# Kernel optimization log

Measured on AMD Instinct MI355X. Metric: run time of the kernel, lower is better.

Reference implementation:

```python
import jax, jax.numpy as jnp
import numpy as np

LN_EPS = 1e-5


def setup_inputs() -> dict:
    key = jax.random.key(0)
    k1, k2, k3, k4, k5, k6 = jax.random.split(key, 6)
    B, S, P = 4, 4096, 16          # batch, seq_len, max_n_bytes
    LR, D = 256, 1024              # lowrank_dim, embedding_dim
    # byte ids in [-1, 255]; -1 marks missing bytes
    bytes_ids = jax.random.randint(k1, (B, S, P), -1, 256)
    byte_table = jax.random.normal(k2, (256, LR), dtype=jnp.float32) * 0.02
    pos_emb = jax.random.normal(k3, (P, LR, LR), dtype=jnp.float32)
    W_up = jax.random.normal(k4, (D, LR), dtype=jnp.float32) * 0.02
    b_up = jnp.zeros((D,), dtype=jnp.float32)
    ln_gamma = jnp.ones((D,), dtype=jnp.float32)
    ln_beta = jnp.zeros((D,), dtype=jnp.float32)
    return {
        "bytes_ids": bytes_ids,
        "byte_table": byte_table,
        "pos_emb": pos_emb,
        "W_up": W_up,
        "b_up": b_up,
        "ln_gamma": ln_gamma,
        "ln_beta": ln_beta,
    }


def reference(bytes_ids, byte_table, pos_emb, W_up, b_up, ln_gamma, ln_beta):
    # bytes_ids: [B, S, P] int, -1 => missing byte
    missing = bytes_ids == -1                             # [B,S,P]
    ids = jnp.where(missing, 0, bytes_ids)
    be = byte_table[ids]                                  # [B,S,P,LR] gather
    # per-position small matmul: pos_emb[p] applied to each byte embedding
    emb = jnp.einsum('pij,bspi->bspj', pos_emb, be)       # [B,S,P,LR]
    emb = jnp.where(missing[..., None], 0.0, emb)         # mask missing bytes
    emb = emb.sum(axis=-2)                                # [B,S,LR]
    x = emb @ W_up.T + b_up                               # [B,S,D]
    # layernorm
    mu = x.mean(axis=-1, keepdims=True)
    var = jnp.mean(jnp.square(x - mu), axis=-1, keepdims=True)
    return (x - mu) * jax.lax.rsqrt(var + LN_EPS) * ln_gamma + ln_beta
```

## Files before the change

### kernel.cpp

```cpp
#include <hip/hip_runtime.h>
#include <stdint.h>

#define PP     16
#define LRDIM  256
#define DDIM   1024
#define LN_EPS 1e-5f

typedef __attribute__((ext_vector_type(8))) short  short8;
typedef __attribute__((ext_vector_type(4))) float  f32x4;

__device__ __forceinline__ uint32_t bf16_rne(float f) {
    uint32_t u = __builtin_bit_cast(uint32_t, f);
    return (u + 0x7fffu + ((u >> 16) & 1u)) >> 16;
}
__device__ __forceinline__ float bf_lo(uint32_t u) {
    return __builtin_bit_cast(float, u << 16);
}
__device__ __forceinline__ float bf_hi(uint32_t u) {
    return __builtin_bit_cast(float, u & 0xffff0000u);
}

__global__ __launch_bounds__(256) void k_table2b(const float* __restrict__ bt,
                                                 const float* __restrict__ pe,
                                                 unsigned short* __restrict__ t2b) {
    const int p  = blockIdx.x >> 6;
    const int c0 = (blockIdx.x & 63) * 4;
    const int j  = threadIdx.x;
    const float* pep = pe + (size_t)p * LRDIM * LRDIM;
    float a0 = 0.f, a1 = 0.f, a2 = 0.f, a3 = 0.f;
    for (int i = 0; i < LRDIM; ++i) {
        float v = pep[i * LRDIM + j];
        a0 += v * bt[(c0 + 0) * LRDIM + i];
        a1 += v * bt[(c0 + 1) * LRDIM + i];
        a2 += v * bt[(c0 + 2) * LRDIM + i];
        a3 += v * bt[(c0 + 3) * LRDIM + i];
    }
    t2b[(size_t)((p * 256) + c0 + 0) * LRDIM + j] = (unsigned short)bf16_rne(a0);
    t2b[(size_t)((p * 256) + c0 + 1) * LRDIM + j] = (unsigned short)bf16_rne(a1);
    t2b[(size_t)((p * 256) + c0 + 2) * LRDIM + j] = (unsigned short)bf16_rne(a2);
    t2b[(size_t)((p * 256) + c0 + 3) * LRDIM + j] = (unsigned short)bf16_rne(a3);
}

__global__ __launch_bounds__(256) void k_wblk(const float* __restrict__ W,
                                              uint4* __restrict__ wb) {
    const int gt  = blockIdx.x * 256 + threadIdx.x;
    const int l   = gt & 63;
    const int ks  = (gt >> 6) & 7;
    const int nfg = gt >> 9;
    const int n   = nfg * 16 + (l & 15);
    const int k   = ks * 32 + (l >> 4) * 8;
    const float* src = W + (size_t)n * LRDIM + k;
    uint32_t r[4];
#pragma unroll
    for (int q = 0; q < 4; ++q) {
        uint32_t lo = bf16_rne(src[2 * q + 0]);
        uint32_t hi = bf16_rne(src[2 * q + 1]);
        r[q] = lo | (hi << 16);
    }
    wb[gt] = make_uint4(r[0], r[1], r[2], r[3]);
}

__global__ __launch_bounds__(256, 2) void k_main(const int* __restrict__ ids,
                                                 const unsigned short* __restrict__ t2b,
                                                 const uint4* __restrict__ wb,
                                                 const float* __restrict__ b_up,
                                                 const float* __restrict__ gamma,
                                                 const float* __restrict__ beta,
                                                 float* __restrict__ out,
                                                 int ntok) {
    __shared__ __align__(16) unsigned char As[32 * 512];
    __shared__ float ln_s[4][32];
    __shared__ float ln_ss[4][32];
    __shared__ int   ids_s[32 * PP];

    const int t    = threadIdx.x;
    const int tok0 = blockIdx.x * 32;
    const int w    = t >> 6;
    const int l    = t & 63;
    const int lo4  = l & 15;
    const int hi2  = l >> 4;

    for (int i = t; i < 32 * PP; i += 256) {
        int tok = tok0 + (i >> 4);
        ids_s[i] = (tok < ntok) ? ids[(size_t)tok0 * PP + i] : -1;
    }
    __syncthreads();

    float av[8][4];
#pragma unroll
    for (int tt = 0; tt < 8; ++tt)
#pragma unroll
        for (int e = 0; e < 4; ++e) av[tt][e] = 0.f;

#pragma unroll
    for (int tt = 0; tt < 8; ++tt) {
        const int tl = (w << 3) + tt;
#pragma unroll 4
        for (int p = 0; p < PP; ++p) {
            const int id = ids_s[tl * PP + p];
            const float msk = (id >= 0) ? 1.f : 0.f;
            const int id2 = id & 255;
            const uint2 vv = *(const uint2*)(t2b + ((size_t)((p << 8) + id2) * LRDIM) + (l << 2));
            av[tt][0] = fmaf(msk, bf_lo(vv.x), av[tt][0]);
            av[tt][1] = fmaf(msk, bf_hi(vv.x), av[tt][1]);
            av[tt][2] = fmaf(msk, bf_lo(vv.y), av[tt][2]);
            av[tt][3] = fmaf(msk, bf_hi(vv.y), av[tt][3]);
        }
    }

#pragma unroll
    for (int tt = 0; tt < 8; ++tt) {
        const int row = (w << 3) + tt;
        uint2 pk;
        pk.x = bf16_rne(av[tt][0]) | (bf16_rne(av[tt][1]) << 16);
        pk.y = bf16_rne(av[tt][2]) | (bf16_rne(av[tt][3]) << 16);
        const int byte = (l << 3) ^ ((row & 7) << 4);
        *(uint2*)(As + (row << 9) + byte) = pk;
    }
    __syncthreads();

    f32x4 acc[2][16];
#pragma unroll
    for (int m2 = 0; m2 < 2; ++m2)
#pragma unroll
        for (int nf = 0; nf < 16; ++nf) {
            f32x4 z = {0.f, 0.f, 0.f, 0.f};
            acc[m2][nf] = z;
        }

#pragma unroll
    for (int ks = 0; ks < 8; ++ks) {
        short8 af[2];
#pragma unroll
        for (int m2 = 0; m2 < 2; ++m2) {
            const int row  = m2 * 16 + lo4;
            const int byte = (ks * 64 + hi2 * 16) ^ ((row & 7) << 4);
            af[m2] = *(const short8*)(As + (row << 9) + byte);
        }
#pragma unroll
        for (int nf = 0; nf < 16; ++nf) {
            const int nfg = (w << 4) + nf;
            const uint4 bv = wb[(size_t)(nfg * 8 + ks) * 64 + l];
            const short8 bf = __builtin_bit_cast(short8, bv);
            acc[0][nf] = __builtin_amdgcn_mfma_f32_16x16x32_bf16(af[0], bf, acc[0][nf], 0, 0, 0);
            acc[1][nf] = __builtin_amdgcn_mfma_f32_16x16x32_bf16(af[1], bf, acc[1][nf], 0, 0, 0);
        }
    }

    float s_[8], ss_[8];
#pragma unroll
    for (int q = 0; q < 8; ++q) { s_[q] = 0.f; ss_[q] = 0.f; }

#pragma unroll
    for (int nf = 0; nf < 16; ++nf) {
        const int col = (w << 8) + (nf << 4) + lo4;
        const float bu = b_up[col];
#pragma unroll
        for (int m2 = 0; m2 < 2; ++m2) {
            f32x4 v = acc[m2][nf];
            v.x += bu; v.y += bu; v.z += bu; v.w += bu;
            acc[m2][nf] = v;
            const int q0 = m2 * 4;
            s_[q0 + 0] += v.x; ss_[q0 + 0] += v.x * v.x;
            s_[q0 + 1] += v.y; ss_[q0 + 1] += v.y * v.y;
            s_[q0 + 2] += v.z; ss_[q0 + 2] += v.z * v.z;
            s_[q0 + 3] += v.w; ss_[q0 + 3] += v.w * v.w;
        }
    }
#pragma unroll
    for (int off = 1; off < 16; off <<= 1)
#pragma unroll
        for (int q = 0; q < 8; ++q) {
            s_[q]  += __shfl_xor(s_[q], off);
            ss_[q] += __shfl_xor(ss_[q], off);
        }
    if (lo4 == 0) {
#pragma unroll
        for (int q = 0; q < 8; ++q) {
            const int tl = (q >> 2) * 16 + hi2 * 4 + (q & 3);
            ln_s[w][tl]  = s_[q];
            ln_ss[w][tl] = ss_[q];
        }
    }
    __syncthreads();

    float mu_[8], inv_[8];
#pragma unroll
    for (int q = 0; q < 8; ++q) {
        const int tl = (q >> 2) * 16 + hi2 * 4 + (q & 3);
        const float S  = ln_s[0][tl] + ln_s[1][tl] + ln_s[2][tl] + ln_s[3][tl];
        const float SS = ln_ss[0][tl] + ln_ss[1][tl] + ln_ss[2][tl] + ln_ss[3][tl];
        const float mu  = S * (1.f / DDIM);
        const float var = SS * (1.f / DDIM) - mu * mu;
        mu_[q]  = mu;
        inv_[q] = rsqrtf(var + LN_EPS);
    }

#pragma unroll
    for (int nf = 0; nf < 16; ++nf) {
        const int col = (w << 8) + (nf << 4) + lo4;
        const float g  = gamma[col];
        const float bb = beta[col];
#pragma unroll
        for (int m2 = 0; m2 < 2; ++m2) {
            const f32x4 v = acc[m2][nf];
#pragma unroll
            for (int r = 0; r < 4; ++r) {
                const int q   = m2 * 4 + r;
                const int tl  = m2 * 16 + hi2 * 4 + r;
                const int tok = tok0 + tl;
                if (tok < ntok)
                    out[(size_t)tok * DDIM + col] = (v[r] - mu_[q]) * inv_[q] * g + bb;
            }
        }
    }
}

extern "C" void kernel_launch(void* const* d_in, const int* in_sizes, int n_in,
                              void* d_out, int out_size, void* d_ws, size_t ws_size,
                              hipStream_t stream) {
    const int*   ids   = (const int*)  d_in[0];
    const float* bt    = (const float*)d_in[1];
    const float* pe    = (const float*)d_in[2];
    const float* W     = (const float*)d_in[3];
    const float* b_up  = (const float*)d_in[4];
    const float* gamma = (const float*)d_in[5];
    const float* beta  = (const float*)d_in[6];
    float* out = (float*)d_out;

    const int ntok = in_sizes[0] / PP;

    char* ws = (char*)d_ws;
    unsigned short* t2b = (unsigned short*)(ws);
    uint4*          wbb = (uint4*)(ws + (2 << 20));

    hipLaunchKernelGGL(k_table2b, dim3(16 * 64), dim3(256), 0, stream, bt, pe, t2b);
    hipLaunchKernelGGL(k_wblk, dim3(128), dim3(256), 0, stream, W, wbb);
    hipLaunchKernelGGL(k_main, dim3((ntok + 31) / 32), dim3(256), 0, stream,
                       ids, t2b, wbb, b_up, gamma, beta, out, ntok);
}
```

Baseline: 79.58 us.

## Split gather from GEMM, merge prep kernels, widen GEMM blocks to 512 threads

Merges the table-precompute and weight-repack kernels into one launch, with the table kernel now computing 8 outputs per thread. The per-token gather moves into its own kernel with one wave per token that writes a bf16 activation matrix to workspace. The GEMM+LayerNorm kernel then reads A directly from global memory, using 512 threads with 8 waves each covering 128 columns. This raises occupancy and parallelism for the gather, at the cost of an extra global round trip for the activations and an additional launch.

```diff
diff --git a/kernel.cpp b/kernel.cpp
--- a/kernel.cpp
+++ b/kernel.cpp
@@ -20,130 +20,120 @@
     return __builtin_bit_cast(float, u & 0xffff0000u);
 }
 
-__global__ __launch_bounds__(256) void k_table2b(const float* __restrict__ bt,
-                                                 const float* __restrict__ pe,
-                                                 unsigned short* __restrict__ t2b) {
-    const int p  = blockIdx.x >> 6;
-    const int c0 = (blockIdx.x & 63) * 4;
-    const int j  = threadIdx.x;
-    const float* pep = pe + (size_t)p * LRDIM * LRDIM;
+__global__ __launch_bounds__(256) void k_prep(const float* __restrict__ bt,
+                                              const float* __restrict__ pe,
+                                              const float* __restrict__ W,
+                                              unsigned short* __restrict__ t2b,
+                                              uint4* __restrict__ wb) {
+    if (blockIdx.x < 512) {
+        const int p  = blockIdx.x >> 5;
+        const int c0 = (blockIdx.x & 31) << 3;
+        const int j  = threadIdx.x;
+        const float* pep = pe + (size_t)p * LRDIM * LRDIM;
+        float a[8];
+#pragma unroll
+        for (int r = 0; r < 8; ++r) a[r] = 0.f;
+#pragma unroll 4
+        for (int i = 0; i < LRDIM; ++i) {
+            const float v = pep[i * LRDIM + j];
+#pragma unroll
+            for (int r = 0; r < 8; ++r)
+                a[r] = fmaf(v, bt[(c0 + r) * LRDIM + i], a[r]);
+        }
+#pragma unroll
+        for (int r = 0; r < 8; ++r)
+            t2b[(size_t)((p << 8) + c0 + r) * LRDIM + j] =
+                (unsigned short)bf16_rne(a[r]);
+    } else {
+        const int gt  = (blockIdx.x - 512) * 256 + threadIdx.x;
+        const int l   = gt & 63;
+        const int ks  = (gt >> 6) & 7;
+        const int nfg = gt >> 9;
+        const int n   = nfg * 16 + (l & 15);
+        const int k   = ks * 32 + (l >> 4) * 8;
+        const float* src = W + (size_t)n * LRDIM + k;
+        uint32_t r[4];
+#pragma unroll
+        for (int q = 0; q < 4; ++q) {
+            const uint32_t lo = bf16_rne(src[2 * q + 0]);
+            const uint32_t hi = bf16_rne(src[2 * q + 1]);
+            r[q] = lo | (hi << 16);
+        }
+        wb[gt] = make_uint4(r[0], r[1], r[2], r[3]);
+    }
+}
+
+__global__ __launch_bounds__(256) void k_gather(const int* __restrict__ ids,
+                                                const unsigned short* __restrict__ t2b,
+                                                uint2* __restrict__ Aq,
+                                                int ntok) {
+    const int wid = (blockIdx.x << 2) + (threadIdx.x >> 6);
+    const int l   = threadIdx.x & 63;
+    if (wid >= ntok) return;
+
+    const int myid = (l < PP) ? ids[(size_t)wid * PP + l] : -1;
+
     float a0 = 0.f, a1 = 0.f, a2 = 0.f, a3 = 0.f;
-    for (int i = 0; i < LRDIM; ++i) {
-        float v = pep[i * LRDIM + j];
-        a0 += v * bt[(c0 + 0) * LRDIM + i];
-        a1 += v * bt[(c0 + 1) * LRDIM + i];
-        a2 += v * bt[(c0 + 2) * LRDIM + i];
-        a3 += v * bt[(c0 + 3) * LRDIM + i];
-    }
-    t2b[(size_t)((p * 256) + c0 + 0) * LRDIM + j] = (unsigned short)bf16_rne(a0);
-    t2b[(size_t)((p * 256) + c0 + 1) * LRDIM + j] = (unsigned short)bf16_rne(a1);
-    t2b[(size_t)((p * 256) + c0 + 2) * LRDIM + j] = (unsigned short)bf16_rne(a2);
-    t2b[(size_t)((p * 256) + c0 + 3) * LRDIM + j] = (unsigned short)bf16_rne(a3);
-}
-
-__global__ __launch_bounds__(256) void k_wblk(const float* __restrict__ W,
-                                              uint4* __restrict__ wb) {
-    const int gt  = blockIdx.x * 256 + threadIdx.x;
-    const int l   = gt & 63;
-    const int ks  = (gt >> 6) & 7;
-    const int nfg = gt >> 9;
-    const int n   = nfg * 16 + (l & 15);
-    const int k   = ks * 32 + (l >> 4) * 8;
-    const float* src = W + (size_t)n * LRDIM + k;
-    uint32_t r[4];
-#pragma unroll
-    for (int q = 0; q < 4; ++q) {
-        uint32_t lo = bf16_rne(src[2 * q + 0]);
-        uint32_t hi = bf16_rne(src[2 * q + 1]);
-        r[q] = lo | (hi << 16);
-    }
-    wb[gt] = make_uint4(r[0], r[1], r[2], r[3]);
-}
-
-__global__ __launch_bounds__(256, 2) void k_main(const int* __restrict__ ids,
-                                                 const unsigned short* __restrict__ t2b,
+#pragma unroll
+    for (int p = 0; p < PP; ++p) {
+        const int   id  = __shfl(myid, p);
+        const float msk = (id >= 0) ? 1.f : 0.f;
+        const uint2 v = *(const uint2*)(t2b +
+                          ((size_t)((p << 8) + (id & 255)) << 8) + (l << 2));
+        a0 = fmaf(msk, bf_lo(v.x), a0);
+        a1 = fmaf(msk, bf_hi(v.x), a1);
+        a2 = fmaf(msk, bf_lo(v.y), a2);
+        a3 = fmaf(msk, bf_hi(v.y), a3);
+    }
+    uint2 pk;
+    pk.x = bf16_rne(a0) | (bf16_rne(a1) << 16);
+    pk.y = bf16_rne(a2) | (bf16_rne(a3) << 16);
+    Aq[(size_t)wid * 64 + l] = pk;
+}
+
+__global__ __launch_bounds__(512, 4) void k_gemm(const unsigned short* __restrict__ A,
                                                  const uint4* __restrict__ wb,
                                                  const float* __restrict__ b_up,
                                                  const float* __restrict__ gamma,
                                                  const float* __restrict__ beta,
                                                  float* __restrict__ out,
                                                  int ntok) {
-    __shared__ __align__(16) unsigned char As[32 * 512];
-    __shared__ float ln_s[4][32];
-    __shared__ float ln_ss[4][32];
-    __shared__ int   ids_s[32 * PP];
+    __shared__ float ln_s[8][32];
+    __shared__ float ln_ss[8][32];
 
     const int t    = threadIdx.x;
-    const int tok0 = blockIdx.x * 32;
     const int w    = t >> 6;
     const int l    = t & 63;
     const int lo4  = l & 15;
     const int hi2  = l >> 4;
-
-    for (int i = t; i < 32 * PP; i += 256) {
-        int tok = tok0 + (i >> 4);
-        ids_s[i] = (tok < ntok) ? ids[(size_t)tok0 * PP + i] : -1;
-    }
-    __syncthreads();
-
-    float av[8][4];
-#pragma unroll
-    for (int tt = 0; tt < 8; ++tt)
-#pragma unroll
-        for (int e = 0; e < 4; ++e) av[tt][e] = 0.f;
-
-#pragma unroll
-    for (int tt = 0; tt < 8; ++tt) {
-        const int tl = (w << 3) + tt;
-#pragma unroll 4
-        for (int p = 0; p < PP; ++p) {
-            const int id = ids_s[tl * PP + p];
-            const float msk = (id >= 0) ? 1.f : 0.f;
-            const int id2 = id & 255;
-            const uint2 vv = *(const uint2*)(t2b + ((size_t)((p << 8) + id2) * LRDIM) + (l << 2));
-            av[tt][0] = fmaf(msk, bf_lo(vv.x), av[tt][0]);
-            av[tt][1] = fmaf(msk, bf_hi(vv.x), av[tt][1]);
-            av[tt][2] = fmaf(msk, bf_lo(vv.y), av[tt][2]);
-            av[tt][3] = fmaf(msk, bf_hi(vv.y), av[tt][3]);
-        }
-    }
-
-#pragma unroll
-    for (int tt = 0; tt < 8; ++tt) {
-        const int row = (w << 3) + tt;
-        uint2 pk;
-        pk.x = bf16_rne(av[tt][0]) | (bf16_rne(av[tt][1]) << 16);
-        pk.y = bf16_rne(av[tt][2]) | (bf16_rne(av[tt][3]) << 16);
-        const int byte = (l << 3) ^ ((row & 7) << 4);
-        *(uint2*)(As + (row << 9) + byte) = pk;
-    }
-    __syncthreads();
-
-    f32x4 acc[2][16];
+    const int tok0 = blockIdx.x << 5;
+
+    f32x4 acc[2][8];
 #pragma unroll
     for (int m2 = 0; m2 < 2; ++m2)
 #pragma unroll
-        for (int nf = 0; nf < 16; ++nf) {
+        for (int nf = 0; nf < 8; ++nf) {
             f32x4 z = {0.f, 0.f, 0.f, 0.f};
             acc[m2][nf] = z;
         }
 
+    const unsigned short* Abase = A + ((size_t)tok0 << 8);
+
 #pragma unroll
     for (int ks = 0; ks < 8; ++ks) {
         short8 af[2];
 #pragma unroll
         for (int m2 = 0; m2 < 2; ++m2) {
-            const int row  = m2 * 16 + lo4;
-            const int byte = (ks * 64 + hi2 * 16) ^ ((row & 7) << 4);
-            af[m2] = *(const short8*)(As + (row << 9) + byte);
-        }
-#pragma unroll
-        for (int nf = 0; nf < 16; ++nf) {
-            const int nfg = (w << 4) + nf;
-            const uint4 bv = wb[(size_t)(nfg * 8 + ks) * 64 + l];
-            const short8 bf = __builtin_bit_cast(short8, bv);
-            acc[0][nf] = __builtin_amdgcn_mfma_f32_16x16x32_bf16(af[0], bf, acc[0][nf], 0, 0, 0);
-            acc[1][nf] = __builtin_amdgcn_mfma_f32_16x16x32_bf16(af[1], bf, acc[1][nf], 0, 0, 0);
+            const int row = (m2 << 4) + lo4;
+            af[m2] = *(const short8*)(Abase + ((size_t)row << 8) + (ks << 5) + (hi2 << 3));
+        }
+#pragma unroll
+        for (int nf = 0; nf < 8; ++nf) {
+            const int nfg = (w << 3) + nf;
+            const uint4 bv = wb[(size_t)((nfg << 3) + ks) * 64 + l];
+            const short8 bfr = __builtin_bit_cast(short8, bv);
+            acc[0][nf] = __builtin_amdgcn_mfma_f32_16x16x32_bf16(af[0], bfr, acc[0][nf], 0, 0, 0);
+            acc[1][nf] = __builtin_amdgcn_mfma_f32_16x16x32_bf16(af[1], bfr, acc[1][nf], 0, 0, 0);
         }
     }
 
@@ -152,8 +142,8 @@
     for (int q = 0; q < 8; ++q) { s_[q] = 0.f; ss_[q] = 0.f; }
 
 #pragma unroll
-    for (int nf = 0; nf < 16; ++nf) {
-        const int col = (w << 8) + (nf << 4) + lo4;
+    for (int nf = 0; nf < 8; ++nf) {
+        const int col = (w << 7) + (nf << 4) + lo4;
         const float bu = b_up[col];
 #pragma unroll
         for (int m2 = 0; m2 < 2; ++m2) {
@@ -188,8 +178,9 @@
 #pragma unroll
     for (int q = 0; q < 8; ++q) {
         const int tl = (q >> 2) * 16 + hi2 * 4 + (q & 3);
-        const float S  = ln_s[0][tl] + ln_s[1][tl] + ln_s[2][tl] + ln_s[3][tl];
-        const float SS = ln_ss[0][tl] + ln_ss[1][tl] + ln_ss[2][tl] + ln_ss[3][tl];
+        float S = 0.f, SS = 0.f;
+#pragma unroll
+        for (int ww = 0; ww < 8; ++ww) { S += ln_s[ww][tl]; SS += ln_ss[ww][tl]; }
         const float mu  = S * (1.f / DDIM);
         const float var = SS * (1.f / DDIM) - mu * mu;
         mu_[q]  = mu;
@@ -197,8 +188,8 @@
     }
 
 #pragma unroll
-    for (int nf = 0; nf < 16; ++nf) {
-        const int col = (w << 8) + (nf << 4) + lo4;
+    for (int nf = 0; nf < 8; ++nf) {
+        const int col = (w << 7) + (nf << 4) + lo4;
         const float g  = gamma[col];
         const float bb = beta[col];
 #pragma unroll
@@ -233,9 +224,12 @@
     char* ws = (char*)d_ws;
     unsigned short* t2b = (unsigned short*)(ws);
     uint4*          wbb = (uint4*)(ws + (2 << 20));
-
-    hipLaunchKernelGGL(k_table2b, dim3(16 * 64), dim3(256), 0, stream, bt, pe, t2b);
-    hipLaunchKernelGGL(k_wblk, dim3(128), dim3(256), 0, stream, W, wbb);
-    hipLaunchKernelGGL(k_main, dim3((ntok + 31) / 32), dim3(256), 0, stream,
-                       ids, t2b, wbb, b_up, gamma, beta, out, ntok);
-}
+    unsigned short* Abf = (unsigned short*)(ws + (3 << 20));
+    uint2*          Aq  = (uint2*)Abf;
+
+    hipLaunchKernelGGL(k_prep, dim3(640), dim3(256), 0, stream, bt, pe, W, t2b, wbb);
+    hipLaunchKernelGGL(k_gather, dim3((ntok + 3) / 4), dim3(256), 0, stream,
+                       ids, t2b, Aq, ntok);
+    hipLaunchKernelGGL(k_gemm, dim3((ntok + 31) / 32), dim3(512), 0, stream,
+                       Abf, wbb, b_up, gamma, beta, out, ntok);
+}
```

Measured after the change: 90.16 us. 13.3% more time.
